# Performance work log

Measured on AMD Instinct MI355X. Metric: run time of the kernel, lower is better.

Reference implementation:

```python
import jax, jax.numpy as jnp
import numpy as np

EPS = 1e-8
NUM_GCN_LAYERS = 2


def _cos(a, b):
    # cosine similarity along last axis, torch.nn.CosineSimilarity semantics
    num = jnp.sum(a * b, axis=-1)
    den = jnp.maximum(jnp.linalg.norm(a, axis=-1) * jnp.linalg.norm(b, axis=-1), EPS)
    return num / den


def _masked_mean(x, mask):
    # x: [..., L, D], mask: [..., L]
    s = jnp.sum(x * mask[..., None], axis=-2)
    d = jnp.maximum(jnp.sum(mask, axis=-1, keepdims=True), 1.0)
    return s / d


def setup_inputs() -> dict:
    key = jax.random.key(0)
    ks = jax.random.split(key, 12)
    B, C, L, D, P, OM, OE, R = 32, 16, 128, 768, 196, 10, 10, 36
    return {
        "mention_text_feature": jax.random.normal(ks[0], (B, L, D), jnp.float32),
        "mention_text_mask": jnp.ones((B, L), jnp.float32),
        "mention_start_pos": jax.random.randint(ks[1], (B,), 0, L),
        "mention_end_pos": jax.random.randint(ks[2], (B,), 0, L),
        "mention_image_feature": jax.random.normal(ks[3], (B, P, D), jnp.float32),
        "mention_object_feature": jax.random.normal(ks[4], (B, OM, R, D), jnp.float32),
        "mention_object_score": jax.random.uniform(ks[5], (B, OM), jnp.float32, 0.1, 1.0),
        "entity_text_feature": jax.random.normal(ks[6], (B, C, L, D), jnp.float32),
        "entity_text_mask": jnp.ones((B, C, L), jnp.float32),
        "entity_image_feature": jax.random.normal(ks[7], (B, C, P, D), jnp.float32),
        "entity_object_feature": jax.random.normal(ks[8], (B, C, OE, R, D), jnp.float32),
        "entity_object_score": jax.random.uniform(ks[9], (B, C, OE), jnp.float32, 0.1, 1.0),
        "miet_similarity": jax.random.normal(ks[10], (B, C), jnp.float32),
        "mtei_similarity": jax.random.normal(ks[11], (B, C), jnp.float32),
    }


def _forward(mtf, mtm, msp, mep, mif, mof, mos, etf, etm, eif, eof, eos, miet, mtei):
    B, L, D = mtf.shape
    C = etf.shape[1]

    # ---- VertexEncoder ----
    v_mt = _masked_mean(mtf, mtm)      # [B, D] mention text vertex
    v_mi = jnp.mean(mif, axis=-2)      # [B, D] mention image vertex
    v_et = _masked_mean(etf, etm)      # [B, C, D] entity text vertex
    v_ei = jnp.mean(eif, axis=-2)      # [B, C, D] entity image vertex

    # ---- EdgeEncoder ----
    # mention final repr: mean of start/end token features (span boundary repr)
    start = jnp.take_along_axis(mtf, msp[:, None, None], axis=1)[:, 0]  # [B, D]
    end = jnp.take_along_axis(mtf, mep[:, None, None], axis=1)[:, 0]    # [B, D]
    m_span = 0.5 * (start + end)
    mtet = _cos(m_span[:, None, :], etf[:, :, 0])  # [B, C] vs entity CLS token

    # miei: the original double python loop over (i, j) object pairs is a
    # weighted average of pairwise cosine sims -> one fused einsum pass.
    m = jnp.mean(mof, axis=-2)         # [B, OM, D]
    e = jnp.mean(eof, axis=-2)         # [B, C, OE, D]
    mn = m / jnp.maximum(jnp.linalg.norm(m, axis=-1, keepdims=True), EPS)
    en = e / jnp.maximum(jnp.linalg.norm(e, axis=-1, keepdims=True), EPS)
    cos_ij = jnp.einsum('bid,bcjd->bcij', mn, en)          # [B, C, OM, OE]
    w = mos[:, None, :, None] * eos[:, :, None, :]          # [B, C, OM, OE]
    miei = jnp.sum(cos_ij * w, axis=(2, 3)) / jnp.sum(w, axis=(2, 3))  # [B, C]

    # ---- GCN layers ----
    edges = [jnp.broadcast_to(x[:, :, None], (B, C, D)) for x in (mtet, mtei, miet, miei)]
    vertexes = [v_mt, v_mi, v_et, v_ei]
    vertex_graph = [[(0, 2), (1, 3)], [(2, 2), (3, 3)], [(0, 0), (2, 1)], [(1, 0), (3, 1)]]
    edge_graph = [(0, 2), (0, 3), (1, 2), (1, 3)]

    def conv_v(edge, v, mention_like):
        msg = edge * (v[:, None, :] if v.ndim == 2 else v)  # [B, C, D]
        return jnp.mean(msg, axis=1) if mention_like else msg

    def conv_e(u, v):
        u2 = u[:, None, :] if u.ndim == 2 else u
        v2 = v[:, None, :] if v.ndim == 2 else v
        return u2 * v2  # [B, C, D]

    for _ in range(NUM_GCN_LAYERS):
        new_v = []
        for k, nbrs in enumerate(vertex_graph):
            mention_like = k < 2  # vertexes 0,1 are [B,D]; 2,3 are [B,C,D]
            acc = conv_v(edges[nbrs[0][0]], vertexes[nbrs[0][1]], mention_like)
            acc = acc + conv_v(edges[nbrs[1][0]], vertexes[nbrs[1][1]], mention_like)
            new_v.append(acc)
        new_e = [conv_e(vertexes[ui], vertexes[vi]) for ui, vi in edge_graph]
        vertexes, edges = new_v, new_e

    mention, entity = vertexes[0], vertexes[2]
    return _cos(mention[:, None, :], entity)  # [B, C]


def reference(mention_text_feature, mention_text_mask, mention_start_pos, mention_end_pos, mention_image_feature, mention_object_feature, mention_object_score, entity_text_feature, entity_text_mask, entity_image_feature, entity_object_feature, entity_object_score, miet_similarity, mtei_similarity):
    return _forward(mention_text_feature, mention_text_mask, mention_start_pos, mention_end_pos, mention_image_feature, mention_object_feature, mention_object_score, entity_text_feature, entity_text_mask, entity_image_feature, entity_object_feature, entity_object_score, miet_similarity, mtei_similarity)
```

## Files before the change

### kernel.cpp

```cpp
#include <hip/hip_runtime.h>

#define EPSF 1e-8f

#define B_  32
#define C_  16
#define L_  128
#define D_  768
#define D4_ 192
#define P_  196
#define OM_ 10
#define OE_ 10
#define R_  36

typedef float f4 __attribute__((ext_vector_type(4)));

__device__ __forceinline__ float f4dot(f4 a, f4 b){ return a.x*b.x + a.y*b.y + a.z*b.z + a.w*b.w; }
__device__ __forceinline__ f4 ldnt(const f4* p){ return __builtin_nontemporal_load(p); }
__device__ __forceinline__ float wave_sum(float v){
  #pragma unroll
  for (int off = 32; off > 0; off >>= 1) v += __shfl_down(v, off);
  return v;
}

__global__ __launch_bounds__(384)
void d1_k(const float* __restrict__ mof, const float* __restrict__ mos,
          const float* __restrict__ mif, const float* __restrict__ mtf,
          const float* __restrict__ mtm, const float* __restrict__ etf,
          const int* __restrict__ msp, const int* __restrict__ mep,
          float* __restrict__ m_mean, float* __restrict__ q,
          float* __restrict__ v_mi, float* __restrict__ v_mt,
          float* __restrict__ mtet)
{
  __shared__ f4 shv[2][D4_];
  __shared__ float shs[4];
  int blk = blockIdx.x, t = threadIdx.x;

  if (blk < 320) {
    int g = blk;
    int half = t / D4_, col = t - half * D4_;
    const f4* base = (const f4*)mof + (size_t)g * R_ * D4_;
    f4 acc = {0.f, 0.f, 0.f, 0.f};
    int r0 = half * 18;
    #pragma unroll 6
    for (int r = r0; r < r0 + 18; ++r) acc += ldnt(base + (size_t)r * D4_ + col);
    shv[half][col] = acc;
    __syncthreads();
    if (t < D4_) {
      f4 mean = (shv[0][col] + shv[1][col]) * (1.f / 36.f);
      ((f4*)m_mean)[(size_t)g * D4_ + col] = mean;
      float n = wave_sum(f4dot(mean, mean));
      if ((t & 63) == 0) shs[t >> 6] = n;
    }
    __syncthreads();
    if (t == 0) q[g] = mos[g] / fmaxf(sqrtf(shs[0] + shs[1] + shs[2]), EPSF);
    return;
  }
  if (blk < 352) {
    int b = blk - 320;
    int half = t / D4_, col = t - half * D4_;
    const f4* base = (const f4*)mif + (size_t)b * P_ * D4_;
    f4 acc = {0.f, 0.f, 0.f, 0.f};
    int r0 = half * 98;
    #pragma unroll 4
    for (int r = r0; r < r0 + 98; ++r) acc += ldnt(base + (size_t)r * D4_ + col);
    shv[half][col] = acc;
    __syncthreads();
    if (t < D4_)
      ((f4*)v_mi)[(size_t)b * D4_ + col] = (shv[0][col] + shv[1][col]) * (1.f / 196.f);
    return;
  }
  if (blk < 384) {
    int b = blk - 352;
    int half = t / D4_, col = t - half * D4_;
    const f4* base = (const f4*)mtf + (size_t)b * L_ * D4_;
    const float* mrow = mtm + (size_t)b * L_;
    f4 acc = {0.f, 0.f, 0.f, 0.f};
    float ms = 0.f;
    int r0 = half * 64;
    #pragma unroll 4
    for (int r = r0; r < r0 + 64; ++r) {
      float w = mrow[r];
      acc += ldnt(base + (size_t)r * D4_ + col) * w;
      ms += w;
    }
    shv[half][col] = acc;
    if (t == 0)    shs[0] = ms;
    if (t == D4_)  shs[1] = ms;
    __syncthreads();
    if (t < D4_) {
      float scale = 1.f / fmaxf(shs[0] + shs[1], 1.f);
      ((f4*)v_mt)[(size_t)b * D4_ + col] = (shv[0][col] + shv[1][col]) * scale;
    }
    return;
  }
  {
    int w = (blk - 384) * 6 + (t >> 6);
    if (w >= B_ * C_) return;
    int lane = t & 63;
    int b = w >> 4;
    const f4* ecls = (const f4*)etf + (size_t)w * L_ * D4_;
    const f4* mb   = (const f4*)mtf + (size_t)b * L_ * D4_;
    int sp = msp[b], ep = mep[b];
    float dt = 0.f, na = 0.f, nb = 0.f;
    #pragma unroll
    for (int k = 0; k < 3; ++k) {
      f4 a = (mb[(size_t)sp * D4_ + lane + 64*k] + mb[(size_t)ep * D4_ + lane + 64*k]) * 0.5f;
      f4 e = ecls[lane + 64*k];
      dt += f4dot(a, e); na += f4dot(a, a); nb += f4dot(e, e);
    }
    dt = wave_sum(dt); na = wave_sum(na); nb = wave_sum(nb);
    if (lane == 0) mtet[w] = dt / fmaxf(sqrtf(na) * sqrtf(nb), EPSF);
  }
}

__global__ __launch_bounds__(192)
void d2_k(const float* __restrict__ eofp, const float* __restrict__ eif,
          const float* __restrict__ etf, const float* __restrict__ etm,
          const float* __restrict__ m_mean, const float* __restrict__ q,
          const float* __restrict__ eos,
          float* __restrict__ part_eif, float* __restrict__ part_etf,
          float* __restrict__ msum_etf, float* __restrict__ p)
{
  int blk = blockIdx.x, t = threadIdx.x;

  if (blk < 1707) {
    int wave = t >> 6, lane = t & 63;
    int g = blk * 3 + wave;
    if (g >= B_ * C_ * OE_) return;
    int b = g / (C_ * OE_);
    const f4* ep = (const f4*)eofp + (size_t)g * R_ * D4_;
    f4 a0 = {0.f,0.f,0.f,0.f}, a1 = a0, a2 = a0;
    #pragma unroll 4
    for (int r = 0; r < R_; ++r) {
      const f4* row = ep + (size_t)r * D4_;
      a0 += ldnt(row + lane);
      a1 += ldnt(row + lane + 64);
      a2 += ldnt(row + lane + 128);
    }
    const float inv36 = 1.f / 36.f;
    a0 *= inv36; a1 *= inv36; a2 *= inv36;
    float nrm = f4dot(a0, a0) + f4dot(a1, a1) + f4dot(a2, a2);
    float s = 0.f;
    const f4* mp = (const f4*)m_mean + (size_t)b * OM_ * D4_;
    #pragma unroll
    for (int i = 0; i < OM_; ++i) {
      const f4* mr = mp + (size_t)i * D4_;
      float di = f4dot(a0, mr[lane]) + f4dot(a1, mr[lane + 64]) + f4dot(a2, mr[lane + 128]);
      s += q[b * OM_ + i] * di;
    }
    s = wave_sum(s); nrm = wave_sum(nrm);
    if (lane == 0) p[g] = eos[g] * s / fmaxf(sqrtf(nrm), EPSF);
    return;
  }
  blk -= 1707;
  if (blk < 1024) {
    int g = blk >> 1, ch = blk & 1;
    const f4* inp = (const f4*)eif + ((size_t)g * P_ + ch * 98) * D4_;
    f4 acc = {0.f,0.f,0.f,0.f};
    #pragma unroll 4
    for (int r = 0; r < 98; ++r) acc += ldnt(inp + (size_t)r * D4_ + t);
    ((f4*)part_eif)[(size_t)blk * D4_ + t] = acc;
    return;
  }
  blk -= 1024;
  {
    int g = blk >> 1, ch = blk & 1;
    const f4* inp = (const f4*)etf + ((size_t)g * L_ + ch * 64) * D4_;
    const float* mrow = etm + (size_t)g * L_ + ch * 64;
    f4 acc = {0.f,0.f,0.f,0.f};
    float ms = 0.f;
    #pragma unroll 4
    for (int r = 0; r < 64; ++r) {
      float w = mrow[r];
      acc += ldnt(inp + (size_t)r * D4_ + t) * w;
      ms += w;
    }
    ((f4*)part_etf)[(size_t)blk * D4_ + t] = acc;
    if (t == 0) msum_etf[blk] = ms;
  }
}

__global__ __launch_bounds__(384)
void d3_k(const float* __restrict__ part_eif, const float* __restrict__ part_etf,
          const float* __restrict__ msum_etf,
          const float* __restrict__ p, const float* __restrict__ mos,
          const float* __restrict__ eos,
          const float* __restrict__ v_mt, const float* __restrict__ v_mi,
          const float* __restrict__ mtet, const float* __restrict__ mtei,
          const float* __restrict__ miet,
          float* __restrict__ out)
{
  __shared__ float s_vet[C_][D_];
  __shared__ float sh_e0[C_], sh_e1[C_], sh_e2[C_], sh_e3[C_];
  __shared__ float sh_m[D_], sh_s[D_];
  int b = blockIdx.x, t = threadIdx.x;

  for (int it = t; it < C_ * D4_; it += 384) {
    int c = it / D4_, col = it - c * D4_;
    int i2 = (b * C_ + c) * 2;
    f4 a = ((const f4*)part_etf)[(size_t)i2 * D4_ + col]
         + ((const f4*)part_etf)[(size_t)(i2 + 1) * D4_ + col];
    float scale = 1.f / fmaxf(msum_etf[i2] + msum_etf[i2 + 1], 1.f);
    ((f4*)&s_vet[c][0])[col] = a * scale;
  }
  if (t < C_) {
    int bc = b * C_ + t;
    float num = 0.f, se = 0.f, sm = 0.f;
    #pragma unroll
    for (int j = 0; j < OE_; ++j) { num += p[bc * OE_ + j]; se += eos[bc * OE_ + j]; }
    #pragma unroll
    for (int i = 0; i < OM_; ++i) sm += mos[b * OM_ + i];
    sh_e3[t] = num / (sm * se);
    sh_e0[t] = mtet[bc];
    sh_e1[t] = mtei[bc];
    sh_e2[t] = miet[bc];
  }
  __syncthreads();

  const float invC = 1.f / (float)C_, inv196 = 1.f / 196.f;
  for (int d = t; d < D_; d += 384) {
    float vmt = v_mt[b * D_ + d], vmi = v_mi[b * D_ + d];
    float nv0 = 0.f, nv1 = 0.f, macc = 0.f;
    #pragma unroll
    for (int c = 0; c < C_; ++c) {
      int i2 = (b * C_ + c) * 2;
      float et = s_vet[c][d];
      float ei = (part_eif[(size_t)i2 * D_ + d] + part_eif[(size_t)(i2 + 1) * D_ + d]) * inv196;
      float e0 = sh_e0[c], e1 = sh_e1[c], e2 = sh_e2[c], e3 = sh_e3[c];
      nv0 += e0 * et + e1 * ei;
      nv1 += e2 * et + e3 * ei;
      macc += (vmt * et) * (e0 * vmt + e2 * vmi)
            + (vmt * ei) * (e1 * vmt + e3 * vmi);
    }
    sh_m[d] = macc * invC;
    sh_s[d] = vmt * (nv0 * invC) + vmi * (nv1 * invC);
  }
  __syncthreads();

  int wv = t >> 6, lane = t & 63;
  for (int c = wv; c < C_; c += 6) {
    const f4* ep = (const f4*)&s_vet[c][0];
    const f4* mp = (const f4*)sh_m;
    const f4* sp = (const f4*)sh_s;
    float dt = 0.f, nm = 0.f, ne = 0.f;
    #pragma unroll
    for (int k = 0; k < 3; ++k) {
      f4 m = mp[lane + 64*k];
      f4 sv = sp[lane + 64*k];
      f4 e = ep[lane + 64*k];
      f4 ent = e * sv;
      dt += f4dot(m, ent); nm += f4dot(m, m); ne += f4dot(ent, ent);
    }
    dt = wave_sum(dt); nm = wave_sum(nm); ne = wave_sum(ne);
    if (lane == 0) out[b * C_ + c] = dt / fmaxf(sqrtf(nm) * sqrtf(ne), EPSF);
  }
}

extern "C" void kernel_launch(void* const* d_in, const int* in_sizes, int n_in,
                              void* d_out, int out_size, void* d_ws, size_t ws_size,
                              hipStream_t stream)
{
  const float* mtf  = (const float*)d_in[0];
  const float* mtm  = (const float*)d_in[1];
  const int*   msp  = (const int*)  d_in[2];
  const int*   mep  = (const int*)  d_in[3];
  const float* mif  = (const float*)d_in[4];
  const float* mof  = (const float*)d_in[5];
  const float* mos  = (const float*)d_in[6];
  const float* etf  = (const float*)d_in[7];
  const float* etm  = (const float*)d_in[8];
  const float* eif  = (const float*)d_in[9];
  const float* eofp = (const float*)d_in[10];
  const float* eos  = (const float*)d_in[11];
  const float* miet = (const float*)d_in[12];
  const float* mtei = (const float*)d_in[13];
  float* out = (float*)d_out;
  float* ws = (float*)d_ws;

  float* PART_EIF = ws;
  float* PART_ETF = PART_EIF + 786432;
  float* MSUM_ETF = PART_ETF + 786432;
  float* M_MEAN   = MSUM_ETF + 2048;
  float* Q        = M_MEAN   + 245760;
  float* V_MT     = Q        + 320;
  float* V_MI     = V_MT     + 24576;
  float* MTET     = V_MI     + 24576;
  float* P_BUF    = MTET     + 512;

  d1_k<<<470, 384, 0, stream>>>(mof, mos, mif, mtf, mtm, etf, msp, mep,
                                M_MEAN, Q, V_MI, V_MT, MTET);

  d2_k<<<3755, 192, 0, stream>>>(eofp, eif, etf, etm, M_MEAN, Q, eos,
                                 PART_EIF, PART_ETF, MSUM_ETF, P_BUF);

  d3_k<<<B_, 384, 0, stream>>>(PART_EIF, PART_ETF, MSUM_ETF, P_BUF, mos, eos,
                               V_MT, V_MI, MTET, mtei, miet, out);
}
```

Baseline: 210.8 us.

## Rebalance kernel stages: move entity text/image reductions into first kernel, split mention reductions

Moves the entity image and entity text partial reductions out of the second kernel into the first, so the second kernel only does the entity object scoring that depends on mention object means. The mention image and text means now become partial sums over more, smaller blocks, and the final kernel reduces those partials into shared memory. The aim is to balance bandwidth-heavy work across the two launches and cut the tail of the small first kernel. In exchange the final kernel does a little more work, and there is more workspace traffic for the partials.

```diff
diff --git a/kernel.cpp b/kernel.cpp
--- a/kernel.cpp
+++ b/kernel.cpp
@@ -22,79 +22,90 @@
   return v;
 }
 
-__global__ __launch_bounds__(384)
-void d1_k(const float* __restrict__ mof, const float* __restrict__ mos,
-          const float* __restrict__ mif, const float* __restrict__ mtf,
-          const float* __restrict__ mtm, const float* __restrict__ etf,
+__global__ __launch_bounds__(192)
+void d1_k(const float* __restrict__ eif, const float* __restrict__ etf,
+          const float* __restrict__ etm, const float* __restrict__ mof,
+          const float* __restrict__ mos, const float* __restrict__ mif,
+          const float* __restrict__ mtf, const float* __restrict__ mtm,
           const int* __restrict__ msp, const int* __restrict__ mep,
+          float* __restrict__ part_eif, float* __restrict__ part_etf,
+          float* __restrict__ msum_etf,
           float* __restrict__ m_mean, float* __restrict__ q,
-          float* __restrict__ v_mi, float* __restrict__ v_mt,
-          float* __restrict__ mtet)
-{
-  __shared__ f4 shv[2][D4_];
-  __shared__ float shs[4];
+          float* __restrict__ part_mif, float* __restrict__ part_mtf,
+          float* __restrict__ msum_mtf, float* __restrict__ mtet)
+{
   int blk = blockIdx.x, t = threadIdx.x;
 
-  if (blk < 320) {
-    int g = blk;
-    int half = t / D4_, col = t - half * D4_;
+  if (blk < 1024) {
+    int g = blk >> 1, ch = blk & 1;
+    const f4* inp = (const f4*)eif + ((size_t)g * P_ + ch * 98) * D4_;
+    f4 acc = {0.f,0.f,0.f,0.f};
+    #pragma unroll 4
+    for (int r = 0; r < 98; ++r) acc += ldnt(inp + (size_t)r * D4_ + t);
+    ((f4*)part_eif)[(size_t)blk * D4_ + t] = acc;
+    return;
+  }
+  if (blk < 2048) {
+    int idx = blk - 1024;
+    int g = idx >> 1, ch = idx & 1;
+    const f4* inp = (const f4*)etf + ((size_t)g * L_ + ch * 64) * D4_;
+    const float* mrow = etm + (size_t)g * L_ + ch * 64;
+    f4 acc = {0.f,0.f,0.f,0.f};
+    float ms = 0.f;
+    #pragma unroll 4
+    for (int r = 0; r < 64; ++r) {
+      float w = mrow[r];
+      acc += ldnt(inp + (size_t)r * D4_ + t) * w;
+      ms += w;
+    }
+    ((f4*)part_etf)[(size_t)idx * D4_ + t] = acc;
+    if (t == 0) msum_etf[idx] = ms;
+    return;
+  }
+  if (blk < 2368) {
+    __shared__ float shs[3];
+    int g = blk - 2048;
     const f4* base = (const f4*)mof + (size_t)g * R_ * D4_;
     f4 acc = {0.f, 0.f, 0.f, 0.f};
-    int r0 = half * 18;
     #pragma unroll 6
-    for (int r = r0; r < r0 + 18; ++r) acc += ldnt(base + (size_t)r * D4_ + col);
-    shv[half][col] = acc;
-    __syncthreads();
-    if (t < D4_) {
-      f4 mean = (shv[0][col] + shv[1][col]) * (1.f / 36.f);
-      ((f4*)m_mean)[(size_t)g * D4_ + col] = mean;
-      float n = wave_sum(f4dot(mean, mean));
-      if ((t & 63) == 0) shs[t >> 6] = n;
-    }
+    for (int r = 0; r < R_; ++r) acc += ldnt(base + (size_t)r * D4_ + t);
+    acc *= (1.f / 36.f);
+    ((f4*)m_mean)[(size_t)g * D4_ + t] = acc;
+    float n = wave_sum(f4dot(acc, acc));
+    if ((t & 63) == 0) shs[t >> 6] = n;
     __syncthreads();
     if (t == 0) q[g] = mos[g] / fmaxf(sqrtf(shs[0] + shs[1] + shs[2]), EPSF);
     return;
   }
-  if (blk < 352) {
-    int b = blk - 320;
-    int half = t / D4_, col = t - half * D4_;
-    const f4* base = (const f4*)mif + (size_t)b * P_ * D4_;
-    f4 acc = {0.f, 0.f, 0.f, 0.f};
-    int r0 = half * 98;
-    #pragma unroll 4
-    for (int r = r0; r < r0 + 98; ++r) acc += ldnt(base + (size_t)r * D4_ + col);
-    shv[half][col] = acc;
-    __syncthreads();
-    if (t < D4_)
-      ((f4*)v_mi)[(size_t)b * D4_ + col] = (shv[0][col] + shv[1][col]) * (1.f / 196.f);
-    return;
-  }
-  if (blk < 384) {
-    int b = blk - 352;
-    int half = t / D4_, col = t - half * D4_;
-    const f4* base = (const f4*)mtf + (size_t)b * L_ * D4_;
-    const float* mrow = mtm + (size_t)b * L_;
-    f4 acc = {0.f, 0.f, 0.f, 0.f};
+  if (blk < 2592) {
+    int idx = blk - 2368;
+    int b = idx / 7, ch = idx - b * 7;
+    const f4* inp = (const f4*)mif + ((size_t)b * P_ + ch * 28) * D4_;
+    f4 acc = {0.f,0.f,0.f,0.f};
+    #pragma unroll 4
+    for (int r = 0; r < 28; ++r) acc += ldnt(inp + (size_t)r * D4_ + t);
+    ((f4*)part_mif)[(size_t)idx * D4_ + t] = acc;
+    return;
+  }
+  if (blk < 2720) {
+    int idx = blk - 2592;
+    int b = idx >> 2, ch = idx & 3;
+    const f4* inp = (const f4*)mtf + ((size_t)b * L_ + ch * 32) * D4_;
+    const float* mrow = mtm + (size_t)b * L_ + ch * 32;
+    f4 acc = {0.f,0.f,0.f,0.f};
     float ms = 0.f;
-    int r0 = half * 64;
-    #pragma unroll 4
-    for (int r = r0; r < r0 + 64; ++r) {
+    #pragma unroll 4
+    for (int r = 0; r < 32; ++r) {
       float w = mrow[r];
-      acc += ldnt(base + (size_t)r * D4_ + col) * w;
+      acc += ldnt(inp + (size_t)r * D4_ + t) * w;
       ms += w;
     }
-    shv[half][col] = acc;
-    if (t == 0)    shs[0] = ms;
-    if (t == D4_)  shs[1] = ms;
-    __syncthreads();
-    if (t < D4_) {
-      float scale = 1.f / fmaxf(shs[0] + shs[1], 1.f);
-      ((f4*)v_mt)[(size_t)b * D4_ + col] = (shv[0][col] + shv[1][col]) * scale;
-    }
+    ((f4*)part_mtf)[(size_t)idx * D4_ + t] = acc;
+    if (t == 0) msum_mtf[idx] = ms;
     return;
   }
   {
-    int w = (blk - 384) * 6 + (t >> 6);
+    int w = (blk - 2720) * 3 + (t >> 6);
     if (w >= B_ * C_) return;
     int lane = t & 63;
     int b = w >> 4;
@@ -114,83 +125,52 @@
 }
 
 __global__ __launch_bounds__(192)
-void d2_k(const float* __restrict__ eofp, const float* __restrict__ eif,
-          const float* __restrict__ etf, const float* __restrict__ etm,
-          const float* __restrict__ m_mean, const float* __restrict__ q,
-          const float* __restrict__ eos,
-          float* __restrict__ part_eif, float* __restrict__ part_etf,
-          float* __restrict__ msum_etf, float* __restrict__ p)
+void d2_k(const float* __restrict__ eofp, const float* __restrict__ m_mean,
+          const float* __restrict__ q, const float* __restrict__ eos,
+          float* __restrict__ p)
 {
   int blk = blockIdx.x, t = threadIdx.x;
-
-  if (blk < 1707) {
-    int wave = t >> 6, lane = t & 63;
-    int g = blk * 3 + wave;
-    if (g >= B_ * C_ * OE_) return;
-    int b = g / (C_ * OE_);
-    const f4* ep = (const f4*)eofp + (size_t)g * R_ * D4_;
-    f4 a0 = {0.f,0.f,0.f,0.f}, a1 = a0, a2 = a0;
-    #pragma unroll 4
-    for (int r = 0; r < R_; ++r) {
-      const f4* row = ep + (size_t)r * D4_;
-      a0 += ldnt(row + lane);
-      a1 += ldnt(row + lane + 64);
-      a2 += ldnt(row + lane + 128);
-    }
-    const float inv36 = 1.f / 36.f;
-    a0 *= inv36; a1 *= inv36; a2 *= inv36;
-    float nrm = f4dot(a0, a0) + f4dot(a1, a1) + f4dot(a2, a2);
-    float s = 0.f;
-    const f4* mp = (const f4*)m_mean + (size_t)b * OM_ * D4_;
-    #pragma unroll
-    for (int i = 0; i < OM_; ++i) {
-      const f4* mr = mp + (size_t)i * D4_;
-      float di = f4dot(a0, mr[lane]) + f4dot(a1, mr[lane + 64]) + f4dot(a2, mr[lane + 128]);
-      s += q[b * OM_ + i] * di;
-    }
-    s = wave_sum(s); nrm = wave_sum(nrm);
-    if (lane == 0) p[g] = eos[g] * s / fmaxf(sqrtf(nrm), EPSF);
-    return;
-  }
-  blk -= 1707;
-  if (blk < 1024) {
-    int g = blk >> 1, ch = blk & 1;
-    const f4* inp = (const f4*)eif + ((size_t)g * P_ + ch * 98) * D4_;
-    f4 acc = {0.f,0.f,0.f,0.f};
-    #pragma unroll 4
-    for (int r = 0; r < 98; ++r) acc += ldnt(inp + (size_t)r * D4_ + t);
-    ((f4*)part_eif)[(size_t)blk * D4_ + t] = acc;
-    return;
-  }
-  blk -= 1024;
-  {
-    int g = blk >> 1, ch = blk & 1;
-    const f4* inp = (const f4*)etf + ((size_t)g * L_ + ch * 64) * D4_;
-    const float* mrow = etm + (size_t)g * L_ + ch * 64;
-    f4 acc = {0.f,0.f,0.f,0.f};
-    float ms = 0.f;
-    #pragma unroll 4
-    for (int r = 0; r < 64; ++r) {
-      float w = mrow[r];
-      acc += ldnt(inp + (size_t)r * D4_ + t) * w;
-      ms += w;
-    }
-    ((f4*)part_etf)[(size_t)blk * D4_ + t] = acc;
-    if (t == 0) msum_etf[blk] = ms;
-  }
+  int wave = t >> 6, lane = t & 63;
+  int g = blk * 3 + wave;
+  if (g >= B_ * C_ * OE_) return;
+  int b = g / (C_ * OE_);
+  const f4* ep = (const f4*)eofp + (size_t)g * R_ * D4_;
+  f4 a0 = {0.f,0.f,0.f,0.f}, a1 = a0, a2 = a0;
+  #pragma unroll 4
+  for (int r = 0; r < R_; ++r) {
+    const f4* row = ep + (size_t)r * D4_;
+    a0 += ldnt(row + lane);
+    a1 += ldnt(row + lane + 64);
+    a2 += ldnt(row + lane + 128);
+  }
+  const float inv36 = 1.f / 36.f;
+  a0 *= inv36; a1 *= inv36; a2 *= inv36;
+  float nrm = f4dot(a0, a0) + f4dot(a1, a1) + f4dot(a2, a2);
+  float s = 0.f;
+  const f4* mp = (const f4*)m_mean + (size_t)b * OM_ * D4_;
+  #pragma unroll
+  for (int i = 0; i < OM_; ++i) {
+    const f4* mr = mp + (size_t)i * D4_;
+    float di = f4dot(a0, mr[lane]) + f4dot(a1, mr[lane + 64]) + f4dot(a2, mr[lane + 128]);
+    s += q[b * OM_ + i] * di;
+  }
+  s = wave_sum(s); nrm = wave_sum(nrm);
+  if (lane == 0) p[g] = eos[g] * s / fmaxf(sqrtf(nrm), EPSF);
 }
 
 __global__ __launch_bounds__(384)
 void d3_k(const float* __restrict__ part_eif, const float* __restrict__ part_etf,
           const float* __restrict__ msum_etf,
+          const float* __restrict__ part_mif, const float* __restrict__ part_mtf,
+          const float* __restrict__ msum_mtf,
           const float* __restrict__ p, const float* __restrict__ mos,
           const float* __restrict__ eos,
-          const float* __restrict__ v_mt, const float* __restrict__ v_mi,
           const float* __restrict__ mtet, const float* __restrict__ mtei,
           const float* __restrict__ miet,
           float* __restrict__ out)
 {
   __shared__ float s_vet[C_][D_];
+  __shared__ float sh_vmt[D_], sh_vmi[D_];
   __shared__ float sh_e0[C_], sh_e1[C_], sh_e2[C_], sh_e3[C_];
   __shared__ float sh_m[D_], sh_s[D_];
   int b = blockIdx.x, t = threadIdx.x;
@@ -203,23 +183,38 @@
     float scale = 1.f / fmaxf(msum_etf[i2] + msum_etf[i2 + 1], 1.f);
     ((f4*)&s_vet[c][0])[col] = a * scale;
   }
-  if (t < C_) {
-    int bc = b * C_ + t;
+  if (t < D4_) {
+    int col = t;
+    f4 a = {0.f,0.f,0.f,0.f};
+    #pragma unroll
+    for (int ch = 0; ch < 4; ++ch)
+      a += ((const f4*)part_mtf)[(size_t)(b * 4 + ch) * D4_ + col];
+    float ms = msum_mtf[b*4] + msum_mtf[b*4+1] + msum_mtf[b*4+2] + msum_mtf[b*4+3];
+    ((f4*)sh_vmt)[col] = a * (1.f / fmaxf(ms, 1.f));
+    f4 v = {0.f,0.f,0.f,0.f};
+    #pragma unroll
+    for (int ch = 0; ch < 7; ++ch)
+      v += ((const f4*)part_mif)[(size_t)(b * 7 + ch) * D4_ + col];
+    ((f4*)sh_vmi)[col] = v * (1.f / 196.f);
+  }
+  if (t >= 256 && t < 256 + C_) {
+    int c = t - 256;
+    int bc = b * C_ + c;
     float num = 0.f, se = 0.f, sm = 0.f;
     #pragma unroll
     for (int j = 0; j < OE_; ++j) { num += p[bc * OE_ + j]; se += eos[bc * OE_ + j]; }
     #pragma unroll
     for (int i = 0; i < OM_; ++i) sm += mos[b * OM_ + i];
-    sh_e3[t] = num / (sm * se);
-    sh_e0[t] = mtet[bc];
-    sh_e1[t] = mtei[bc];
-    sh_e2[t] = miet[bc];
+    sh_e3[c] = num / (sm * se);
+    sh_e0[c] = mtet[bc];
+    sh_e1[c] = mtei[bc];
+    sh_e2[c] = miet[bc];
   }
   __syncthreads();
 
   const float invC = 1.f / (float)C_, inv196 = 1.f / 196.f;
   for (int d = t; d < D_; d += 384) {
-    float vmt = v_mt[b * D_ + d], vmi = v_mi[b * D_ + d];
+    float vmt = sh_vmt[d], vmi = sh_vmi[d];
     float nv0 = 0.f, nv1 = 0.f, macc = 0.f;
     #pragma unroll
     for (int c = 0; c < C_; ++c) {
@@ -280,19 +275,22 @@
   float* PART_EIF = ws;
   float* PART_ETF = PART_EIF + 786432;
   float* MSUM_ETF = PART_ETF + 786432;
-  float* M_MEAN   = MSUM_ETF + 2048;
+  float* PART_MIF = MSUM_ETF + 1024;
+  float* PART_MTF = PART_MIF + 172032;
+  float* MSUM_MTF = PART_MTF + 98304;
+  float* M_MEAN   = MSUM_MTF + 128;
   float* Q        = M_MEAN   + 245760;
-  float* V_MT     = Q        + 320;
-  float* V_MI     = V_MT     + 24576;
-  float* MTET     = V_MI     + 24576;
+  float* MTET     = Q        + 320;
   float* P_BUF    = MTET     + 512;
 
-  d1_k<<<470, 384, 0, stream>>>(mof, mos, mif, mtf, mtm, etf, msp, mep,
-                                M_MEAN, Q, V_MI, V_MT, MTET);
-
-  d2_k<<<3755, 192, 0, stream>>>(eofp, eif, etf, etm, M_MEAN, Q, eos,
-                                 PART_EIF, PART_ETF, MSUM_ETF, P_BUF);
-
-  d3_k<<<B_, 384, 0, stream>>>(PART_EIF, PART_ETF, MSUM_ETF, P_BUF, mos, eos,
-                               V_MT, V_MI, MTET, mtei, miet, out);
-}
+  d1_k<<<2891, 192, 0, stream>>>(eif, etf, etm, mof, mos, mif, mtf, mtm,
+                                 msp, mep,
+                                 PART_EIF, PART_ETF, MSUM_ETF,
+                                 M_MEAN, Q, PART_MIF, PART_MTF, MSUM_MTF, MTET);
+
+  d2_k<<<1707, 192, 0, stream>>>(eofp, M_MEAN, Q, eos, P_BUF);
+
+  d3_k<<<B_, 384, 0, stream>>>(PART_EIF, PART_ETF, MSUM_ETF,
+                               PART_MIF, PART_MTF, MSUM_MTF,
+                               P_BUF, mos, eos, MTET, mtei, miet, out);
+}
```

New measurement: 194.0 us. 1.09x faster.
